# Performance work log

Measured on AMD Instinct MI355X. Metric: run time of the kernel, lower is better.

## Reference

```python
import jax, jax.numpy as jnp
import numpy as np
import math

INV = 1.0 / (2.0 * math.pi) ** 2  # 1/(2*pi)^2 normalization used throughout
EPS = 1e-8


def setup_inputs() -> dict:
    key = jax.random.key(0)
    ks = jax.random.split(key, 5)
    N, K, J = 512, 8, 6
    return {
        "x_hat": jax.random.normal(ks[0], (N, N, 2), jnp.float32),
        "phi_hat_real": jax.random.normal(ks[1], (N, N), jnp.float32),
        "phi_hat_imag": jax.random.normal(ks[2], (N, N), jnp.float32),
        "psi_hat_real": jax.random.normal(ks[3], (K, J, N, N), jnp.float32),
        "psi_hat_imag": jax.random.normal(ks[4], (K, J, N, N), jnp.float32),
    }


def reference(x_hat, phi_hat_real, phi_hat_imag, psi_hat_real, psi_hat_imag):
    K, J, N, _ = psi_hat_real.shape
    NN = N * N
    phi2 = phi_hat_real ** 2 + phi_hat_imag ** 2  # [N,N]

    # zeroth-order coefficient: full spatial mean of |x_hat|^2 * |phi_hat|^2
    s0 = INV * jnp.mean((x_hat[:, :, 0] ** 2 + x_hat[:, :, 1] ** 2) * phi2)

    # first layer: complex multiply in Fourier domain, ifft2, modulus, fft2
    xc = jax.lax.complex(x_hat[:, :, 0], x_hat[:, :, 1])          # [N,N] complex
    psic = jax.lax.complex(psi_hat_real, psi_hat_imag)            # [K,J,N,N] complex
    temp = jnp.fft.ifft2(xc[None, None] * psic, axes=(-2, -1))    # [K,J,N,N] complex
    mod = jnp.sqrt(temp.real ** 2 + temp.imag ** 2 + EPS)         # modulus nonlinearity
    t2 = jnp.fft.fft2(mod, axes=(-2, -1))                         # rfft onesided=False == full fft of real
    power = (t2.real ** 2 + t2.imag ** 2).reshape(K, J, NN)       # |U1_hat|^2

    # first-order coefficients a[k,i] = INV * mean(power * phi2)
    a = INV * (power @ phi2.reshape(NN)) / NN                     # [K,J]

    # second-order coefficients via GEMM over spatial dim:
    # B[k,i,m,j] = INV * mean_xy(power[k,i] * |psi[m,j]|^2)
    psi2 = (psi_hat_real ** 2 + psi_hat_imag ** 2).reshape(K, J, NN)
    B = INV * jnp.einsum('kin,mjn->kimj', power, psi2) / NN       # [K,J,K,J]

    # assemble output in the same concatenation order as the torch loop:
    # [s0, a_0, b_0(flattened over k,m,j'), a_1, b_1, ..., a_{J-1}]
    pieces = [s0[None]]
    for i in range(J):
        pieces.append(a[:, i])
        if i < J - 1:
            pieces.append(B[:, i, :, i + 1:J].reshape(-1))
    return jnp.concatenate(pieces, axis=0)
```

## Files before the change

### kernel.cpp

```cpp
#include <hip/hip_runtime.h>
#include <hip/hip_fp16.h>

#define Nn 512
#define NNe 262144
#define CST 546

__device__ __forceinline__ float2 f2(float x, float y){ return make_float2(x, y); }
__device__ __forceinline__ float2 cadd(float2 a, float2 b){ return f2(a.x+b.x, a.y+b.y); }
__device__ __forceinline__ float2 csub(float2 a, float2 b){ return f2(a.x-b.x, a.y-b.y); }
__device__ __forceinline__ float2 cmul(float2 a, float2 b){
    return f2(a.x*b.x - a.y*b.y, a.x*b.y + a.y*b.x);
}
__device__ __forceinline__ int pidx(int p){ return p + (p>>4) + (p>>7); }
#define WFENCE() __builtin_amdgcn_wave_barrier()

template<int SGN>
__device__ __forceinline__ void fft8(float2 a[8]){
    const float r = 0.7071067811865476f;
    const float S = (float)SGN;
    float2 u0 = cadd(a[0], a[4]), u1 = cadd(a[1], a[5]);
    float2 u2 = cadd(a[2], a[6]), u3 = cadd(a[3], a[7]);
    float2 v0 = csub(a[0], a[4]), v1 = csub(a[1], a[5]);
    float2 v2 = csub(a[2], a[6]), v3 = csub(a[3], a[7]);
    v1 = cmul(v1, f2(r, S*r));
    v2 = cmul(v2, f2(0.f, S));
    v3 = cmul(v3, f2(-r, S*r));
    float2 p0 = cadd(u0, u2), p1 = cadd(u1, u3);
    float2 q0 = csub(u0, u2), q1 = cmul(csub(u1, u3), f2(0.f, S));
    a[0] = cadd(p0, p1); a[4] = csub(p0, p1);
    a[2] = cadd(q0, q1); a[6] = csub(q0, q1);
    p0 = cadd(v0, v2); p1 = cadd(v1, v3);
    q0 = csub(v0, v2); q1 = cmul(csub(v1, v3), f2(0.f, S));
    a[1] = cadd(p0, p1); a[5] = csub(p0, p1);
    a[3] = cadd(q0, q1); a[7] = csub(q0, q1);
}

template<int SGN>
__device__ __forceinline__ float2 twd(int idx, float inv){
    float ang = ((float)SGN) * 6.283185307179586f * (inv * (float)idx);
    float s, c;
    __sincosf(ang, &s, &c);
    return f2(c, s);
}

template<int SGN>
__device__ void fft512_dif(float2 v[8], float2* buf, int lane){
    fft8<SGN>(v);
    {
        float2 w1 = twd<SGN>(lane, 1.f/512.f);
        float2 w  = f2(1.f, 0.f);
        #pragma unroll
        for (int r = 0; r < 8; ++r){
            buf[pidx(r*64 + lane)] = cmul(v[r], w);
            w = cmul(w, w1);
        }
    }
    WFENCE();
    int rb = (lane >> 3) * 64, t2 = lane & 7;
    float2 y[8];
    #pragma unroll
    for (int q = 0; q < 8; ++q) y[q] = buf[pidx(rb + t2 + 8*q)];
    fft8<SGN>(y);
    WFENCE();
    {
        float2 w2 = twd<SGN>(t2, 1.f/64.f);
        float2 w  = f2(1.f, 0.f);
        #pragma unroll
        for (int r = 0; r < 8; ++r){
            buf[pidx(rb + r*8 + t2)] = cmul(y[r], w);
            w = cmul(w, w2);
        }
    }
    WFENCE();
    int base = rb + t2*8;
    #pragma unroll
    for (int q = 0; q < 8; ++q) v[q] = buf[pidx(base + q)];
    fft8<SGN>(v);
}

template<int SGN>
__device__ void fft512_dit(float2 v[8], float2* buf, int lane){
    int rb = (lane >> 3) * 64, t2 = lane & 7;
    fft8<SGN>(v);
    int base = rb + t2*8;
    #pragma unroll
    for (int q = 0; q < 8; ++q) buf[pidx(base + q)] = v[q];
    WFENCE();
    float2 y[8];
    #pragma unroll
    for (int r = 0; r < 8; ++r) y[r] = buf[pidx(rb + r*8 + t2)];
    {
        float2 w2 = twd<SGN>(t2, 1.f/64.f);
        float2 w  = f2(1.f, 0.f);
        #pragma unroll
        for (int r = 0; r < 8; ++r){
            y[r] = cmul(y[r], w);
            w = cmul(w, w2);
        }
    }
    fft8<SGN>(y);
    WFENCE();
    #pragma unroll
    for (int q = 0; q < 8; ++q) buf[pidx(rb + t2 + 8*q)] = y[q];
    WFENCE();
    #pragma unroll
    for (int r = 0; r < 8; ++r) v[r] = buf[pidx(r*64 + lane)];
    {
        float2 w1 = twd<SGN>(lane, 1.f/512.f);
        float2 w  = f2(1.f, 0.f);
        #pragma unroll
        for (int r = 0; r < 8; ++r){
            v[r] = cmul(v[r], w);
            w = cmul(w, w1);
        }
    }
    fft8<SGN>(v);
}

__global__ __launch_bounds__(256, 6)
void k_mulrow(const float2* __restrict__ xh, const float* __restrict__ pr,
              const float* __restrict__ pi, __half2* __restrict__ temp,
              __half* __restrict__ psi2h){
    __shared__ float2 lds[4][548];
    int wave = threadIdx.x >> 6, lane = threadIdx.x & 63;
    int img  = blockIdx.x >> 7;
    int row  = ((blockIdx.x & 127) << 2) | wave;
    size_t boff = (size_t)img * NNe + (size_t)row * Nn;
    const float2* xr = xh + (size_t)row * Nn;
    float2 v[8];
    #pragma unroll
    for (int q = 0; q < 8; ++q){
        int x = lane + 64*q;
        float2 xv = xr[x];
        float2 pv = f2(pr[boff + x], pi[boff + x]);
        psi2h[boff + x] = __float2half_rn(pv.x*pv.x + pv.y*pv.y);
        v[q] = cmul(xv, pv);
    }
    fft512_dif<1>(v, lds[wave], lane);
    __half2* outp = temp + boff;
    #pragma unroll
    for (int q = 0; q < 8; ++q) outp[64*q + lane] = __floats2half2_rn(v[q].x, v[q].y);
}

__global__ __launch_bounds__(512, 6)
void k_colfused(__half2* __restrict__ temp){
    __shared__ float2 tile[8 * CST];
    int img = blockIdx.x >> 6;
    int x0  = (blockIdx.x & 63) << 3;
    __half2* srcH = temp + (size_t)img * NNe + x0;
    for (int i = threadIdx.x; i < 1024; i += 512){
        int yy = i >> 1, c4 = (i & 1) << 2;
        uint4 u = *(const uint4*)&srcH[(size_t)yy * Nn + c4];
        tile[(c4+0)*CST + pidx(yy)] = __half22float2(*(__half2*)&u.x);
        tile[(c4+1)*CST + pidx(yy)] = __half22float2(*(__half2*)&u.y);
        tile[(c4+2)*CST + pidx(yy)] = __half22float2(*(__half2*)&u.z);
        tile[(c4+3)*CST + pidx(yy)] = __half22float2(*(__half2*)&u.w);
    }
    __syncthreads();
    int wave = threadIdx.x >> 6, lane = threadIdx.x & 63;
    const float sc = 3.814697265625e-06f;
    {
        float2* buf = &tile[wave * CST];
        float2 v[8];
        #pragma unroll
        for (int q = 0; q < 8; ++q) v[q] = buf[pidx(lane + 64*q)];
        fft512_dif<1>(v, buf, lane);
        #pragma unroll
        for (int q = 0; q < 8; ++q){
            float re = v[q].x * sc, im = v[q].y * sc;
            v[q] = f2(sqrtf(re*re + im*im + 1e-8f), 0.f);
        }
        WFENCE();
        fft512_dit<-1>(v, buf, lane);
        #pragma unroll
        for (int q = 0; q < 8; ++q) buf[pidx(lane + 64*q)] = v[q];
    }
    __syncthreads();
    for (int i = threadIdx.x; i < 1024; i += 512){
        int yy = i >> 1, c4 = (i & 1) << 2;
        uint4 u;
        float2 a0 = tile[(c4+0)*CST + pidx(yy)];
        float2 a1 = tile[(c4+1)*CST + pidx(yy)];
        float2 a2 = tile[(c4+2)*CST + pidx(yy)];
        float2 a3 = tile[(c4+3)*CST + pidx(yy)];
        *(__half2*)&u.x = __floats2half2_rn(a0.x, a0.y);
        *(__half2*)&u.y = __floats2half2_rn(a1.x, a1.y);
        *(__half2*)&u.z = __floats2half2_rn(a2.x, a2.y);
        *(__half2*)&u.w = __floats2half2_rn(a3.x, a3.y);
        *(uint4*)&srcH[(size_t)yy * Nn + c4] = u;
    }
}

__global__ __launch_bounds__(256, 6)
void k_rowpow(const __half2* __restrict__ temp, __half* __restrict__ powerh){
    __shared__ float2 lds[4][548];
    int wave = threadIdx.x >> 6, lane = threadIdx.x & 63;
    int img  = blockIdx.x >> 7;
    int row  = ((blockIdx.x & 127) << 2) | wave;
    const __half2* src = temp + (size_t)img * NNe + (size_t)row * Nn;
    float2 v[8];
    #pragma unroll
    for (int q = 0; q < 8; ++q) v[q] = __half22float2(src[64*q + lane]);
    fft512_dit<-1>(v, lds[wave], lane);
    __half* dst = powerh + (size_t)img * NNe + (size_t)row * Nn;
    #pragma unroll
    for (int q = 0; q < 8; ++q)
        dst[lane + 64*q] = __float2half_rn((v[q].x*v[q].x + v[q].y*v[q].y) * 0.00390625f);
}

__global__ __launch_bounds__(256)
void k_s0(const float2* __restrict__ xh, const float* __restrict__ phr,
          const float* __restrict__ phii, float* __restrict__ part){
    int gid = blockIdx.x*256 + threadIdx.x;
    float acc = 0.f;
    for (int n = gid; n < NNe; n += 256*256){
        float2 x = xh[n];
        float a = phr[n], b = phii[n];
        acc += (x.x*x.x + x.y*x.y) * (a*a + b*b);
    }
    #pragma unroll
    for (int o = 32; o > 0; o >>= 1) acc += __shfl_down(acc, o, 64);
    __shared__ float wsum[4];
    int wave = threadIdx.x >> 6, lane = threadIdx.x & 63;
    if (lane == 0) wsum[wave] = acc;
    __syncthreads();
    if (threadIdx.x == 0) part[blockIdx.x] = wsum[0]+wsum[1]+wsum[2]+wsum[3];
}

__global__ __launch_bounds__(128)
void k_gemm(const __half* __restrict__ powerh, const __half* __restrict__ psi2h,
            const float* __restrict__ phr, const float* __restrict__ phii,
            float* __restrict__ partC){
    __shared__ __align__(16) float P[2][48][68];
    __shared__ __align__(16) float W[2][56][68];
    int wave = threadIdx.x >> 6, lane = threadIdx.x & 63;
    float (*Pw)[68] = P[wave];
    float (*Ww)[68] = W[wave];
    int gw = blockIdx.x*2 + wave;
    int lm = lane >> 3, lw = lane & 7;
    float acc[6][7] = {};
    #pragma unroll
    for (int r = 49; r < 56; ++r){
        Ww[r][lane] = 0.f;
        if (lane < 4) Ww[r][64 + lane] = 0.f;
    }
    int n0 = gw * 256;
    for (int st = 0; st < 4; ++st){
        int nb = n0 + st*64;
        __syncthreads();
        #pragma unroll
        for (int rr = 0; rr < 12; ++rr){
            int row = rr*4 + (lane >> 4);
            int c4  = (lane & 15) * 4;
            size_t off = (size_t)row*NNe + nb + c4;
            const __half2* p2 = (const __half2*)&powerh[off];
            float2 f0 = __half22float2(p2[0]);
            float2 f1 = __half22float2(p2[1]);
            *(float4*)&Pw[row][c4] = make_float4(f0.x, f0.y, f1.x, f1.y);
        }
        #pragma unroll
        for (int rr = 0; rr < 12; ++rr){
            int row = rr*4 + (lane >> 4);
            int c4  = (lane & 15) * 4;
            size_t off = (size_t)row*NNe + nb + c4;
            const __half2* p2 = (const __half2*)&psi2h[off];
            float2 f0 = __half22float2(p2[0]);
            float2 f1 = __half22float2(p2[1]);
            *(float4*)&Ww[row][c4] = make_float4(f0.x, f0.y, f1.x, f1.y);
        }
        if (lane < 16){
            int c4 = lane * 4;
            float4 a = *(const float4*)&phr[nb + c4];
            float4 b = *(const float4*)&phii[nb + c4];
            float4 w4;
            w4.x = a.x*a.x + b.x*b.x; w4.y = a.y*a.y + b.y*b.y;
            w4.z = a.z*a.z + b.z*b.z; w4.w = a.w*a.w + b.w*b.w;
            *(float4*)&Ww[48][c4] = w4;
        }
        __syncthreads();
        #pragma unroll 2
        for (int nn = 0; nn < 64; nn += 4){
            float4 pa[6], wb[7];
            #pragma unroll
            for (int i = 0; i < 6; ++i) pa[i] = *(const float4*)&Pw[lm + 8*i][nn];
            #pragma unroll
            for (int j = 0; j < 7; ++j) wb[j] = *(const float4*)&Ww[lw + 8*j][nn];
            #pragma unroll
            for (int i = 0; i < 6; ++i)
                #pragma unroll
                for (int j = 0; j < 7; ++j){
                    float s = acc[i][j];
                    s = fmaf(pa[i].x, wb[j].x, s);
                    s = fmaf(pa[i].y, wb[j].y, s);
                    s = fmaf(pa[i].z, wb[j].z, s);
                    s = fmaf(pa[i].w, wb[j].w, s);
                    acc[i][j] = s;
                }
        }
    }
    float* outp = partC + (size_t)gw * 2400;
    #pragma unroll
    for (int i = 0; i < 6; ++i)
        #pragma unroll
        for (int j = 0; j < 7; ++j){
            int m = lm + 8*i, wc = lw + 8*j;
            if (wc < 49) outp[m*50 + wc] = acc[i][j];
        }
}

__global__ __launch_bounds__(256)
void k_redc1(const float* __restrict__ partC, float* __restrict__ partC2){
    __shared__ float red[4][64];
    int es = threadIdx.x & 63, wave = threadIdx.x >> 6;
    int e = blockIdx.x*64 + es;
    int b0 = blockIdx.y*64 + wave*16;
    float s = 0.f;
    if (e < 2400){
        #pragma unroll
        for (int u = 0; u < 16; ++u) s += partC[(size_t)(b0+u)*2400 + e];
    }
    red[wave][es] = s;
    __syncthreads();
    if (wave == 0 && e < 2400)
        partC2[(size_t)blockIdx.y*2400 + e] = red[0][es]+red[1][es]+red[2][es]+red[3][es];
}
__global__ __launch_bounds__(256)
void k_redc2(const float* __restrict__ partC2, float* __restrict__ CF){
    __shared__ float red[4][64];
    int es = threadIdx.x & 63, wave = threadIdx.x >> 6;
    int e = blockIdx.x*64 + es;
    float s = 0.f;
    if (e < 2400){
        #pragma unroll
        for (int u = 0; u < 4; ++u) s += partC2[(size_t)(wave*4+u)*2400 + e];
    }
    red[wave][es] = s;
    __syncthreads();
    if (wave == 0 && e < 2400)
        CF[e] = red[0][es]+red[1][es]+red[2][es]+red[3][es];
}

__global__ __launch_bounds__(256)
void k_final(const float* __restrict__ CF, const float* __restrict__ partS0,
             float* __restrict__ outp, float SC0, float SCC){
    __shared__ float ssum[4];
    int tid = threadIdx.x, wave = tid >> 6, lane = tid & 63;
    float a = partS0[tid];
    #pragma unroll
    for (int o = 32; o > 0; o >>= 1) a += __shfl_down(a, o, 64);
    if (lane == 0) ssum[wave] = a;
    __syncthreads();
    if (tid == 0) outp[0] = SC0 * (ssum[0]+ssum[1]+ssum[2]+ssum[3]);
    int off = 1;
    for (int i = 0; i < 6; ++i){
        if (tid < 8) outp[off + tid] = SCC * CF[(tid*6 + i)*50 + 48];
        off += 8;
        if (i < 5){
            int nj = 5 - i, cnt = 64 * nj;
            for (int p = tid; p < cnt; p += 256){
                int j2 = p % nj;
                int km = p / nj;
                int m = km & 7, k = km >> 3;
                outp[off + p] = SCC * CF[(k*6 + i)*50 + m*6 + (i + 1 + j2)];
            }
            off += cnt;
        }
    }
}

extern "C" void kernel_launch(void* const* d_in, const int* in_sizes, int n_in,
                              void* d_out, int out_size, void* d_ws, size_t ws_size,
                              hipStream_t stream){
    (void)in_sizes; (void)n_in; (void)out_size; (void)ws_size;
    const float2* xh  = (const float2*)d_in[0];
    const float*  phr = (const float*)d_in[1];
    const float*  phi_= (const float*)d_in[2];
    const float*  psr = (const float*)d_in[3];
    const float*  psi_= (const float*)d_in[4];
    float* outp = (float*)d_out;
    float* ws   = (float*)d_ws;

    size_t o_power = 0;
    size_t o_partC = o_power + (size_t)24 * NNe;
    size_t o_pC2   = o_partC + (size_t)1024 * 2400;
    size_t o_s0    = o_pC2 + (size_t)16 * 2400;
    size_t o_CF    = o_s0 + 256;
    size_t o_temp  = o_CF + 2400;
    size_t o_psi2  = o_temp + (size_t)48 * NNe;
    __half*  powerh= (__half*)(ws + o_power);
    float*   partC = ws + o_partC;
    float*   partC2= ws + o_pC2;
    float*   ps0   = ws + o_s0;
    float*   CF    = ws + o_CF;
    __half2* temp  = (__half2*)(ws + o_temp);
    __half*  psi2h = (__half*)(ws + o_psi2);

    const double INVd = 1.0 / (4.0 * 3.14159265358979323846 * 3.14159265358979323846);
    const float SC0 = (float)(INVd / (double)NNe);
    const float SCC = (float)(INVd / (double)NNe * 256.0);

    k_s0<<<dim3(256), dim3(256), 0, stream>>>(xh, phr, phi_, ps0);
    k_mulrow<<<dim3(48*128), dim3(256), 0, stream>>>(xh, psr, psi_, temp, psi2h);
    k_colfused<<<dim3(48*64), dim3(512), 0, stream>>>(temp);
    k_rowpow<<<dim3(48*128), dim3(256), 0, stream>>>(temp, powerh);
    k_gemm<<<dim3(512), dim3(128), 0, stream>>>(powerh, psi2h, phr, phi_, partC);
    k_redc1<<<dim3(38, 16), dim3(256), 0, stream>>>(partC, partC2);
    k_redc2<<<dim3(38), dim3(256), 0, stream>>>(partC2, CF);
    k_final<<<dim3(1), dim3(256), 0, stream>>>(CF, ps0, outp, SC0, SCC);
}
```

Before: 158.2 us.

## Tile intermediate FFT buffer column-blocked, precompute twiddle tables, relax GEMM syncs

Stores the intermediate half-precision spectrum in a column-tiled layout (8-column tiles of 4096 elements). The column-FFT kernel can then read and write each tile contiguously, and the row kernels stage their rows through shared memory to produce 16-byte coalesced accesses. Twiddle factors are now computed once per thread into register tables shared by the forward and inverse passes, where before each pass recomputed them by recurrence. The block barriers in the GEMM staging loop become wave barriers because each wave uses only its own LDS region. Launch bounds for the row kernels drop to 4 to make room for the extra shared memory and registers.

Result: slower. 192.4 us (+21.6%).

```diff
diff --git a/kernel.cpp b/kernel.cpp
--- a/kernel.cpp
+++ b/kernel.cpp
@@ -35,26 +35,35 @@
     a[3] = cadd(q0, q1); a[7] = csub(q0, q1);
 }
 
-template<int SGN>
-__device__ __forceinline__ float2 twd(int idx, float inv){
-    float ang = ((float)SGN) * 6.283185307179586f * (inv * (float)idx);
+__device__ __forceinline__ float2 twdp(int idx, float inv){
+    float ang = 6.283185307179586f * (inv * (float)idx);
     float s, c;
     __sincosf(ang, &s, &c);
     return f2(c, s);
 }
 
 template<int SGN>
-__device__ void fft512_dif(float2 v[8], float2* buf, int lane){
+__device__ __forceinline__ float2 applyw(float2 a, float2 w){
+    return (SGN > 0) ? f2(a.x*w.x - a.y*w.y, a.x*w.y + a.y*w.x)
+                     : f2(a.x*w.x + a.y*w.y, a.y*w.x - a.x*w.y);
+}
+
+__device__ __forceinline__ void make_tw(int lane, float2 tw1[8], float2 tw2[8]){
+    tw1[0] = f2(1.f, 0.f); tw1[1] = twdp(lane, 1.f/512.f);
+    #pragma unroll
+    for (int r = 2; r < 8; ++r) tw1[r] = cmul(tw1[r-1], tw1[1]);
+    tw2[0] = f2(1.f, 0.f); tw2[1] = twdp(lane & 7, 1.f/64.f);
+    #pragma unroll
+    for (int r = 2; r < 8; ++r) tw2[r] = cmul(tw2[r-1], tw2[1]);
+}
+
+template<int SGN>
+__device__ void fft512_dif(float2 v[8], float2* buf, int lane,
+                           const float2 tw1[8], const float2 tw2[8]){
     fft8<SGN>(v);
-    {
-        float2 w1 = twd<SGN>(lane, 1.f/512.f);
-        float2 w  = f2(1.f, 0.f);
-        #pragma unroll
-        for (int r = 0; r < 8; ++r){
-            buf[pidx(r*64 + lane)] = cmul(v[r], w);
-            w = cmul(w, w1);
-        }
-    }
+    #pragma unroll
+    for (int r = 0; r < 8; ++r)
+        buf[pidx(r*64 + lane)] = applyw<SGN>(v[r], tw1[r]);
     WFENCE();
     int rb = (lane >> 3) * 64, t2 = lane & 7;
     float2 y[8];
@@ -62,15 +71,9 @@
     for (int q = 0; q < 8; ++q) y[q] = buf[pidx(rb + t2 + 8*q)];
     fft8<SGN>(y);
     WFENCE();
-    {
-        float2 w2 = twd<SGN>(t2, 1.f/64.f);
-        float2 w  = f2(1.f, 0.f);
-        #pragma unroll
-        for (int r = 0; r < 8; ++r){
-            buf[pidx(rb + r*8 + t2)] = cmul(y[r], w);
-            w = cmul(w, w2);
-        }
-    }
+    #pragma unroll
+    for (int r = 0; r < 8; ++r)
+        buf[pidx(rb + r*8 + t2)] = applyw<SGN>(y[r], tw2[r]);
     WFENCE();
     int base = rb + t2*8;
     #pragma unroll
@@ -79,7 +82,8 @@
 }
 
 template<int SGN>
-__device__ void fft512_dit(float2 v[8], float2* buf, int lane){
+__device__ void fft512_dit(float2 v[8], float2* buf, int lane,
+                           const float2 tw1[8], const float2 tw2[8]){
     int rb = (lane >> 3) * 64, t2 = lane & 7;
     fft8<SGN>(v);
     int base = rb + t2*8;
@@ -89,15 +93,8 @@
     float2 y[8];
     #pragma unroll
     for (int r = 0; r < 8; ++r) y[r] = buf[pidx(rb + r*8 + t2)];
-    {
-        float2 w2 = twd<SGN>(t2, 1.f/64.f);
-        float2 w  = f2(1.f, 0.f);
-        #pragma unroll
-        for (int r = 0; r < 8; ++r){
-            y[r] = cmul(y[r], w);
-            w = cmul(w, w2);
-        }
-    }
+    #pragma unroll
+    for (int r = 0; r < 8; ++r) y[r] = applyw<SGN>(y[r], tw2[r]);
     fft8<SGN>(y);
     WFENCE();
     #pragma unroll
@@ -105,26 +102,24 @@
     WFENCE();
     #pragma unroll
     for (int r = 0; r < 8; ++r) v[r] = buf[pidx(r*64 + lane)];
-    {
-        float2 w1 = twd<SGN>(lane, 1.f/512.f);
-        float2 w  = f2(1.f, 0.f);
-        #pragma unroll
-        for (int r = 0; r < 8; ++r){
-            v[r] = cmul(v[r], w);
-            w = cmul(w, w1);
-        }
-    }
+    #pragma unroll
+    for (int r = 0; r < 8; ++r) v[r] = applyw<SGN>(v[r], tw1[r]);
     fft8<SGN>(v);
 }
 
-__global__ __launch_bounds__(256, 6)
+
+__global__ __launch_bounds__(256, 4)
 void k_mulrow(const float2* __restrict__ xh, const float* __restrict__ pr,
               const float* __restrict__ pi, __half2* __restrict__ temp,
               __half* __restrict__ psi2h){
     __shared__ float2 lds[4][548];
+    __shared__ __half2 h2out[4][520];
     int wave = threadIdx.x >> 6, lane = threadIdx.x & 63;
     int img  = blockIdx.x >> 7;
-    int row  = ((blockIdx.x & 127) << 2) | wave;
+    int y0   = ((blockIdx.x & 127) << 2);
+    int row  = y0 | wave;
+    float2 tw1[8], tw2[8];
+    make_tw(lane, tw1, tw2);
     size_t boff = (size_t)img * NNe + (size_t)row * Nn;
     const float2* xr = xh + (size_t)row * Nn;
     float2 v[8];
@@ -136,73 +131,103 @@
         psi2h[boff + x] = __float2half_rn(pv.x*pv.x + pv.y*pv.y);
         v[q] = cmul(xv, pv);
     }
-    fft512_dif<1>(v, lds[wave], lane);
-    __half2* outp = temp + boff;
-    #pragma unroll
-    for (int q = 0; q < 8; ++q) outp[64*q + lane] = __floats2half2_rn(v[q].x, v[q].y);
+    fft512_dif<1>(v, lds[wave], lane, tw1, tw2);
+    #pragma unroll
+    for (int q = 0; q < 8; ++q)
+        h2out[wave][64*q + lane] = __floats2half2_rn(v[q].x, v[q].y);
+    __syncthreads();
+    __half2* base = temp + (size_t)img * NNe;
+    #pragma unroll
+    for (int it = 0; it < 2; ++it){
+        int idx = it*256 + threadIdx.x;
+        int ct = idx >> 3, rr = (idx >> 1) & 3, h = idx & 1;
+        uint4 u = *(const uint4*)&h2out[rr][ct*8 + h*4];
+        *(uint4*)&base[(size_t)ct*4096 + (size_t)(y0 + rr)*8 + h*4] = u;
+    }
 }
 
 __global__ __launch_bounds__(512, 6)
 void k_colfused(__half2* __restrict__ temp){
     __shared__ float2 tile[8 * CST];
     int img = blockIdx.x >> 6;
-    int x0  = (blockIdx.x & 63) << 3;
-    __half2* srcH = temp + (size_t)img * NNe + x0;
-    for (int i = threadIdx.x; i < 1024; i += 512){
-        int yy = i >> 1, c4 = (i & 1) << 2;
-        uint4 u = *(const uint4*)&srcH[(size_t)yy * Nn + c4];
-        tile[(c4+0)*CST + pidx(yy)] = __half22float2(*(__half2*)&u.x);
-        tile[(c4+1)*CST + pidx(yy)] = __half22float2(*(__half2*)&u.y);
-        tile[(c4+2)*CST + pidx(yy)] = __half22float2(*(__half2*)&u.z);
-        tile[(c4+3)*CST + pidx(yy)] = __half22float2(*(__half2*)&u.w);
+    int ct  = blockIdx.x & 63;
+    __half2* gbase = temp + (size_t)img * NNe + (size_t)ct * 4096;
+    #pragma unroll
+    for (int it = 0; it < 2; ++it){
+        int u = it*512 + threadIdx.x;
+        int r = u >> 1, cb = (u & 1) << 2;
+        uint4 w = *(const uint4*)&gbase[u*4];
+        tile[(cb+0)*CST + pidx(r)] = __half22float2(*(__half2*)&w.x);
+        tile[(cb+1)*CST + pidx(r)] = __half22float2(*(__half2*)&w.y);
+        tile[(cb+2)*CST + pidx(r)] = __half22float2(*(__half2*)&w.z);
+        tile[(cb+3)*CST + pidx(r)] = __half22float2(*(__half2*)&w.w);
     }
     __syncthreads();
     int wave = threadIdx.x >> 6, lane = threadIdx.x & 63;
+    float2 tw1[8], tw2[8];
+    make_tw(lane, tw1, tw2);
     const float sc = 3.814697265625e-06f;
     {
         float2* buf = &tile[wave * CST];
         float2 v[8];
         #pragma unroll
         for (int q = 0; q < 8; ++q) v[q] = buf[pidx(lane + 64*q)];
-        fft512_dif<1>(v, buf, lane);
+        fft512_dif<1>(v, buf, lane, tw1, tw2);
         #pragma unroll
         for (int q = 0; q < 8; ++q){
             float re = v[q].x * sc, im = v[q].y * sc;
             v[q] = f2(sqrtf(re*re + im*im + 1e-8f), 0.f);
         }
         WFENCE();
-        fft512_dit<-1>(v, buf, lane);
+        fft512_dit<-1>(v, buf, lane, tw1, tw2);
         #pragma unroll
         for (int q = 0; q < 8; ++q) buf[pidx(lane + 64*q)] = v[q];
     }
     __syncthreads();
-    for (int i = threadIdx.x; i < 1024; i += 512){
-        int yy = i >> 1, c4 = (i & 1) << 2;
-        uint4 u;
-        float2 a0 = tile[(c4+0)*CST + pidx(yy)];
-        float2 a1 = tile[(c4+1)*CST + pidx(yy)];
-        float2 a2 = tile[(c4+2)*CST + pidx(yy)];
-        float2 a3 = tile[(c4+3)*CST + pidx(yy)];
-        *(__half2*)&u.x = __floats2half2_rn(a0.x, a0.y);
-        *(__half2*)&u.y = __floats2half2_rn(a1.x, a1.y);
-        *(__half2*)&u.z = __floats2half2_rn(a2.x, a2.y);
-        *(__half2*)&u.w = __floats2half2_rn(a3.x, a3.y);
-        *(uint4*)&srcH[(size_t)yy * Nn + c4] = u;
-    }
-}
-
-__global__ __launch_bounds__(256, 6)
+    #pragma unroll
+    for (int it = 0; it < 2; ++it){
+        int u = it*512 + threadIdx.x;
+        int r = u >> 1, cb = (u & 1) << 2;
+        uint4 w;
+        float2 a0 = tile[(cb+0)*CST + pidx(r)];
+        float2 a1 = tile[(cb+1)*CST + pidx(r)];
+        float2 a2 = tile[(cb+2)*CST + pidx(r)];
+        float2 a3 = tile[(cb+3)*CST + pidx(r)];
+        *(__half2*)&w.x = __floats2half2_rn(a0.x, a0.y);
+        *(__half2*)&w.y = __floats2half2_rn(a1.x, a1.y);
+        *(__half2*)&w.z = __floats2half2_rn(a2.x, a2.y);
+        *(__half2*)&w.w = __floats2half2_rn(a3.x, a3.y);
+        *(uint4*)&gbase[u*4] = w;
+    }
+}
+
+__global__ __launch_bounds__(256, 4)
 void k_rowpow(const __half2* __restrict__ temp, __half* __restrict__ powerh){
     __shared__ float2 lds[4][548];
+    __shared__ float2 rows[4][520];
     int wave = threadIdx.x >> 6, lane = threadIdx.x & 63;
     int img  = blockIdx.x >> 7;
-    int row  = ((blockIdx.x & 127) << 2) | wave;
-    const __half2* src = temp + (size_t)img * NNe + (size_t)row * Nn;
+    int y0   = ((blockIdx.x & 127) << 2);
+    const __half2* base = temp + (size_t)img * NNe;
+    #pragma unroll
+    for (int it = 0; it < 2; ++it){
+        int idx = it*256 + threadIdx.x;
+        int ct = idx >> 3, rr = (idx >> 1) & 3, h = idx & 1;
+        uint4 u = *(const uint4*)&base[(size_t)ct*4096 + (size_t)(y0 + rr)*8 + h*4];
+        int s = ct*8 + h*4;
+        rows[rr][s+0] = __half22float2(*(__half2*)&u.x);
+        rows[rr][s+1] = __half22float2(*(__half2*)&u.y);
+        rows[rr][s+2] = __half22float2(*(__half2*)&u.z);
+        rows[rr][s+3] = __half22float2(*(__half2*)&u.w);
+    }
+    __syncthreads();
+    float2 tw1[8], tw2[8];
+    make_tw(lane, tw1, tw2);
     float2 v[8];
     #pragma unroll
-    for (int q = 0; q < 8; ++q) v[q] = __half22float2(src[64*q + lane]);
-    fft512_dit<-1>(v, lds[wave], lane);
-    __half* dst = powerh + (size_t)img * NNe + (size_t)row * Nn;
+    for (int q = 0; q < 8; ++q) v[q] = rows[wave][64*q + lane];
+    fft512_dit<-1>(v, lds[wave], lane, tw1, tw2);
+    __half* dst = powerh + (size_t)img * NNe + (size_t)(y0 + wave) * Nn;
     #pragma unroll
     for (int q = 0; q < 8; ++q)
         dst[lane + 64*q] = __float2half_rn((v[q].x*v[q].x + v[q].y*v[q].y) * 0.00390625f);
@@ -247,7 +272,7 @@
     int n0 = gw * 256;
     for (int st = 0; st < 4; ++st){
         int nb = n0 + st*64;
-        __syncthreads();
+        WFENCE();
         #pragma unroll
         for (int rr = 0; rr < 12; ++rr){
             int row = rr*4 + (lane >> 4);
@@ -277,7 +302,7 @@
             w4.z = a.z*a.z + b.z*b.z; w4.w = a.w*a.w + b.w*b.w;
             *(float4*)&Ww[48][c4] = w4;
         }
-        __syncthreads();
+        WFENCE();
         #pragma unroll 2
         for (int nn = 0; nn < 64; nn += 4){
             float4 pa[6], wb[7];
```

## Write column-FFT output transposed, stage row reads in LDS, merge final reductions

Applied to the files above, without the earlier changes.

The column kernel no longer copies its tile back through LDS into the original layout. It writes each column's result directly as a contiguous row of a new transposed buffer. The row-power kernel then gathers 16-byte chunks from that buffer into LDS before its FFT. Block barriers in the GEMM staging loop are replaced with wave-only barriers, and the second reduction kernel is folded into the final single-block kernel to save a launch. The trade-offs are strided 16-byte global reads in the row kernel and an extra workspace buffer. The wave barrier in the GEMM is only safe if each wave uses its own LDS region.

After: 188.0 us. 18.8% more time.

```diff
diff --git a/kernel.cpp b/kernel.cpp
--- a/kernel.cpp
+++ b/kernel.cpp
@@ -35,19 +35,19 @@
     a[3] = cadd(q0, q1); a[7] = csub(q0, q1);
 }
 
-template<int SGN>
-__device__ __forceinline__ float2 twd(int idx, float inv){
-    float ang = ((float)SGN) * 6.283185307179586f * (inv * (float)idx);
+__device__ __forceinline__ float2 twdp(int idx, float inv){
+    float ang = 6.283185307179586f * (inv * (float)idx);
     float s, c;
     __sincosf(ang, &s, &c);
     return f2(c, s);
 }
 
 template<int SGN>
-__device__ void fft512_dif(float2 v[8], float2* buf, int lane){
+__device__ void fft512_dif_i(float2 v[8], float2* buf, int lane){
     fft8<SGN>(v);
     {
-        float2 w1 = twd<SGN>(lane, 1.f/512.f);
+        float2 w1 = twdp(lane, 1.f/512.f);
+        if (SGN < 0) w1.y = -w1.y;
         float2 w  = f2(1.f, 0.f);
         #pragma unroll
         for (int r = 0; r < 8; ++r){
@@ -63,7 +63,8 @@
     fft8<SGN>(y);
     WFENCE();
     {
-        float2 w2 = twd<SGN>(t2, 1.f/64.f);
+        float2 w2 = twdp(t2, 1.f/64.f);
+        if (SGN < 0) w2.y = -w2.y;
         float2 w  = f2(1.f, 0.f);
         #pragma unroll
         for (int r = 0; r < 8; ++r){
@@ -79,7 +80,7 @@
 }
 
 template<int SGN>
-__device__ void fft512_dit(float2 v[8], float2* buf, int lane){
+__device__ void fft512_dit_i(float2 v[8], float2* buf, int lane){
     int rb = (lane >> 3) * 64, t2 = lane & 7;
     fft8<SGN>(v);
     int base = rb + t2*8;
@@ -90,7 +91,8 @@
     #pragma unroll
     for (int r = 0; r < 8; ++r) y[r] = buf[pidx(rb + r*8 + t2)];
     {
-        float2 w2 = twd<SGN>(t2, 1.f/64.f);
+        float2 w2 = twdp(t2, 1.f/64.f);
+        if (SGN < 0) w2.y = -w2.y;
         float2 w  = f2(1.f, 0.f);
         #pragma unroll
         for (int r = 0; r < 8; ++r){
@@ -106,7 +108,8 @@
     #pragma unroll
     for (int r = 0; r < 8; ++r) v[r] = buf[pidx(r*64 + lane)];
     {
-        float2 w1 = twd<SGN>(lane, 1.f/512.f);
+        float2 w1 = twdp(lane, 1.f/512.f);
+        if (SGN < 0) w1.y = -w1.y;
         float2 w  = f2(1.f, 0.f);
         #pragma unroll
         for (int r = 0; r < 8; ++r){
@@ -136,18 +139,18 @@
         psi2h[boff + x] = __float2half_rn(pv.x*pv.x + pv.y*pv.y);
         v[q] = cmul(xv, pv);
     }
-    fft512_dif<1>(v, lds[wave], lane);
+    fft512_dif_i<1>(v, lds[wave], lane);
     __half2* outp = temp + boff;
     #pragma unroll
     for (int q = 0; q < 8; ++q) outp[64*q + lane] = __floats2half2_rn(v[q].x, v[q].y);
 }
 
 __global__ __launch_bounds__(512, 6)
-void k_colfused(__half2* __restrict__ temp){
+void k_colfused(const __half2* __restrict__ temp, __half2* __restrict__ temp2){
     __shared__ float2 tile[8 * CST];
     int img = blockIdx.x >> 6;
     int x0  = (blockIdx.x & 63) << 3;
-    __half2* srcH = temp + (size_t)img * NNe + x0;
+    const __half2* srcH = temp + (size_t)img * NNe + x0;
     for (int i = threadIdx.x; i < 1024; i += 512){
         int yy = i >> 1, c4 = (i & 1) << 2;
         uint4 u = *(const uint4*)&srcH[(size_t)yy * Nn + c4];
@@ -159,50 +162,46 @@
     __syncthreads();
     int wave = threadIdx.x >> 6, lane = threadIdx.x & 63;
     const float sc = 3.814697265625e-06f;
-    {
-        float2* buf = &tile[wave * CST];
-        float2 v[8];
-        #pragma unroll
-        for (int q = 0; q < 8; ++q) v[q] = buf[pidx(lane + 64*q)];
-        fft512_dif<1>(v, buf, lane);
-        #pragma unroll
-        for (int q = 0; q < 8; ++q){
-            float re = v[q].x * sc, im = v[q].y * sc;
-            v[q] = f2(sqrtf(re*re + im*im + 1e-8f), 0.f);
-        }
-        WFENCE();
-        fft512_dit<-1>(v, buf, lane);
-        #pragma unroll
-        for (int q = 0; q < 8; ++q) buf[pidx(lane + 64*q)] = v[q];
-    }
-    __syncthreads();
-    for (int i = threadIdx.x; i < 1024; i += 512){
-        int yy = i >> 1, c4 = (i & 1) << 2;
-        uint4 u;
-        float2 a0 = tile[(c4+0)*CST + pidx(yy)];
-        float2 a1 = tile[(c4+1)*CST + pidx(yy)];
-        float2 a2 = tile[(c4+2)*CST + pidx(yy)];
-        float2 a3 = tile[(c4+3)*CST + pidx(yy)];
-        *(__half2*)&u.x = __floats2half2_rn(a0.x, a0.y);
-        *(__half2*)&u.y = __floats2half2_rn(a1.x, a1.y);
-        *(__half2*)&u.z = __floats2half2_rn(a2.x, a2.y);
-        *(__half2*)&u.w = __floats2half2_rn(a3.x, a3.y);
-        *(uint4*)&srcH[(size_t)yy * Nn + c4] = u;
-    }
+    float2* buf = &tile[wave * CST];
+    float2 v[8];
+    #pragma unroll
+    for (int q = 0; q < 8; ++q) v[q] = buf[pidx(lane + 64*q)];
+    fft512_dif_i<1>(v, buf, lane);
+    #pragma unroll
+    for (int q = 0; q < 8; ++q){
+        float re = v[q].x * sc, im = v[q].y * sc;
+        v[q] = f2(sqrtf(re*re + im*im + 1e-8f), 0.f);
+    }
+    WFENCE();
+    fft512_dit_i<-1>(v, buf, lane);
+    __half2* dst = temp2 + (size_t)img * NNe + (size_t)(x0 + wave) * Nn;
+    #pragma unroll
+    for (int q = 0; q < 8; ++q) dst[lane + 64*q] = __floats2half2_rn(v[q].x, v[q].y);
 }
 
 __global__ __launch_bounds__(256, 6)
-void k_rowpow(const __half2* __restrict__ temp, __half* __restrict__ powerh){
+void k_rowpow(const __half2* __restrict__ temp2, __half* __restrict__ powerh){
     __shared__ float2 lds[4][548];
+    __shared__ __half2 st[4][520];
     int wave = threadIdx.x >> 6, lane = threadIdx.x & 63;
     int img  = blockIdx.x >> 7;
-    int row  = ((blockIdx.x & 127) << 2) | wave;
-    const __half2* src = temp + (size_t)img * NNe + (size_t)row * Nn;
+    int y0   = ((blockIdx.x & 127) << 2);
+    const __half2* base = temp2 + (size_t)img * NNe;
+    #pragma unroll
+    for (int it = 0; it < 2; ++it){
+        int s = it*256 + threadIdx.x;
+        uint4 u = *(const uint4*)&base[(size_t)s * Nn + y0];
+        st[0][s] = *(__half2*)&u.x;
+        st[1][s] = *(__half2*)&u.y;
+        st[2][s] = *(__half2*)&u.z;
+        st[3][s] = *(__half2*)&u.w;
+    }
+    __syncthreads();
     float2 v[8];
     #pragma unroll
-    for (int q = 0; q < 8; ++q) v[q] = __half22float2(src[64*q + lane]);
-    fft512_dit<-1>(v, lds[wave], lane);
-    __half* dst = powerh + (size_t)img * NNe + (size_t)row * Nn;
+    for (int q = 0; q < 8; ++q) v[q] = __half22float2(st[wave][64*q + lane]);
+    fft512_dit_i<-1>(v, lds[wave], lane);
+    __half* dst = powerh + (size_t)img * NNe + (size_t)(y0 + wave) * Nn;
     #pragma unroll
     for (int q = 0; q < 8; ++q)
         dst[lane + 64*q] = __float2half_rn((v[q].x*v[q].x + v[q].y*v[q].y) * 0.00390625f);
@@ -247,7 +246,7 @@
     int n0 = gw * 256;
     for (int st = 0; st < 4; ++st){
         int nb = n0 + st*64;
-        __syncthreads();
+        WFENCE();
         #pragma unroll
         for (int rr = 0; rr < 12; ++rr){
             int row = rr*4 + (lane >> 4);
@@ -277,7 +276,7 @@
             w4.z = a.z*a.z + b.z*b.z; w4.w = a.w*a.w + b.w*b.w;
             *(float4*)&Ww[48][c4] = w4;
         }
-        __syncthreads();
+        WFENCE();
         #pragma unroll 2
         for (int nn = 0; nn < 64; nn += 4){
             float4 pa[6], wb[7];
@@ -324,27 +323,19 @@
     if (wave == 0 && e < 2400)
         partC2[(size_t)blockIdx.y*2400 + e] = red[0][es]+red[1][es]+red[2][es]+red[3][es];
 }
+
 __global__ __launch_bounds__(256)
-void k_redc2(const float* __restrict__ partC2, float* __restrict__ CF){
-    __shared__ float red[4][64];
-    int es = threadIdx.x & 63, wave = threadIdx.x >> 6;
-    int e = blockIdx.x*64 + es;
-    float s = 0.f;
-    if (e < 2400){
-        #pragma unroll
-        for (int u = 0; u < 4; ++u) s += partC2[(size_t)(wave*4+u)*2400 + e];
-    }
-    red[wave][es] = s;
-    __syncthreads();
-    if (wave == 0 && e < 2400)
-        CF[e] = red[0][es]+red[1][es]+red[2][es]+red[3][es];
-}
-
-__global__ __launch_bounds__(256)
-void k_final(const float* __restrict__ CF, const float* __restrict__ partS0,
+void k_final(const float* __restrict__ partC2, const float* __restrict__ partS0,
              float* __restrict__ outp, float SC0, float SCC){
+    __shared__ float CFs[2400];
     __shared__ float ssum[4];
     int tid = threadIdx.x, wave = tid >> 6, lane = tid & 63;
+    for (int e = tid; e < 2400; e += 256){
+        float s = 0.f;
+        #pragma unroll
+        for (int u = 0; u < 16; ++u) s += partC2[(size_t)u*2400 + e];
+        CFs[e] = SCC * s;
+    }
     float a = partS0[tid];
     #pragma unroll
     for (int o = 32; o > 0; o >>= 1) a += __shfl_down(a, o, 64);
@@ -353,7 +344,7 @@
     if (tid == 0) outp[0] = SC0 * (ssum[0]+ssum[1]+ssum[2]+ssum[3]);
     int off = 1;
     for (int i = 0; i < 6; ++i){
-        if (tid < 8) outp[off + tid] = SCC * CF[(tid*6 + i)*50 + 48];
+        if (tid < 8) outp[off + tid] = CFs[(tid*6 + i)*50 + 48];
         off += 8;
         if (i < 5){
             int nj = 5 - i, cnt = 64 * nj;
@@ -361,7 +352,7 @@
                 int j2 = p % nj;
                 int km = p / nj;
                 int m = km & 7, k = km >> 3;
-                outp[off + p] = SCC * CF[(k*6 + i)*50 + m*6 + (i + 1 + j2)];
+                outp[off + p] = CFs[(k*6 + i)*50 + m*6 + (i + 1 + j2)];
             }
             off += cnt;
         }
@@ -384,16 +375,16 @@
     size_t o_partC = o_power + (size_t)24 * NNe;
     size_t o_pC2   = o_partC + (size_t)1024 * 2400;
     size_t o_s0    = o_pC2 + (size_t)16 * 2400;
-    size_t o_CF    = o_s0 + 256;
-    size_t o_temp  = o_CF + 2400;
+    size_t o_temp  = o_s0 + 256;
     size_t o_psi2  = o_temp + (size_t)48 * NNe;
+    size_t o_temp2 = o_psi2 + (size_t)24 * NNe;
     __half*  powerh= (__half*)(ws + o_power);
     float*   partC = ws + o_partC;
     float*   partC2= ws + o_pC2;
     float*   ps0   = ws + o_s0;
-    float*   CF    = ws + o_CF;
     __half2* temp  = (__half2*)(ws + o_temp);
     __half*  psi2h = (__half*)(ws + o_psi2);
+    __half2* temp2 = (__half2*)(ws + o_temp2);
 
     const double INVd = 1.0 / (4.0 * 3.14159265358979323846 * 3.14159265358979323846);
     const float SC0 = (float)(INVd / (double)NNe);
@@ -401,10 +392,9 @@
 
     k_s0<<<dim3(256), dim3(256), 0, stream>>>(xh, phr, phi_, ps0);
     k_mulrow<<<dim3(48*128), dim3(256), 0, stream>>>(xh, psr, psi_, temp, psi2h);
-    k_colfused<<<dim3(48*64), dim3(512), 0, stream>>>(temp);
-    k_rowpow<<<dim3(48*128), dim3(256), 0, stream>>>(temp, powerh);
+    k_colfused<<<dim3(48*64), dim3(512), 0, stream>>>(temp, temp2);
+    k_rowpow<<<dim3(48*128), dim3(256), 0, stream>>>(temp2, powerh);
     k_gemm<<<dim3(512), dim3(128), 0, stream>>>(powerh, psi2h, phr, phi_, partC);
     k_redc1<<<dim3(38, 16), dim3(256), 0, stream>>>(partC, partC2);
-    k_redc2<<<dim3(38), dim3(256), 0, stream>>>(partC2, CF);
-    k_final<<<dim3(1), dim3(256), 0, stream>>>(CF, ps0, outp, SC0, SCC);
-}
+    k_final<<<dim3(1), dim3(256), 0, stream>>>(partC2, ps0, outp, SC0, SCC);
+}
```
